# Kernel optimization log

Hardware: AMD Instinct MI355X
Metric: run time of the kernel (lower is better)

Reference implementation:

```python
import jax, jax.numpy as jnp
import numpy as np

NPOINT = 1024   # npoint
K = 20          # num_samples[0]


def _fps(pts, npoint):
    """Iterative furthest point sampling. pts: [N,3] -> indices [npoint] (starts at idx 0)."""
    N = pts.shape[0]

    def step(carry, _):
        min_d, last = carry
        d = jnp.sum((pts - pts[last]) ** 2, axis=-1)          # [N] dist to last selected
        min_d = jnp.minimum(min_d, d)                          # running min-dist to selected set
        nxt = jnp.argmax(min_d).astype(jnp.int32)
        return (min_d, nxt), nxt

    init = (jnp.full((N,), 1e10, pts.dtype), jnp.int32(0))
    _, rest = jax.lax.scan(step, init, None, length=npoint - 1)
    return jnp.concatenate([jnp.zeros((1,), jnp.int32), rest])


def _pdist2(q, p):
    """Squared pairwise distances. q:[M,3], p:[N,3] -> [M,N], clamped to >=0 (matches pdist2squared)."""
    d = jnp.sum(q * q, -1)[:, None] + jnp.sum(p * p, -1)[None, :] - 2.0 * (q @ p.T)
    return jnp.maximum(d, 0.0)


def _knn(q, p, k):
    """k nearest neighbors of each q among p, dropping the closest (self), ascending order."""
    d = _pdist2(q, p)                       # [M,N]
    _, idx = jax.lax.top_k(-d, k + 1)       # ascending distance order
    return idx[:, 1:]                       # drop self, [M,k]


def setup_inputs() -> dict:
    key = jax.random.key(0)
    points = jax.random.normal(key, (4, 16384, 3), dtype=jnp.float32)
    return {"points": points}


def reference(points):
    B, N, _ = points.shape
    # --- FPS node sampling (Sample module) ---
    xyz_ind = jax.vmap(lambda p: _fps(p, NPOINT))(points)                  # [B, N1]
    xyz_query = jnp.take_along_axis(points, xyz_ind[:, :, None], axis=1)  # [B, N1, 3]

    # --- Gmid: neighbors of the N1 query points among all N points ---
    nbr_mid = jax.vmap(lambda q, p: _knn(q, p, K))(xyz_query, points)      # [B, N1, K]
    src_mid = jnp.take_along_axis(points, nbr_mid.reshape(B, -1, 1), axis=1).reshape(B, NPOINT, K, 3)
    d_mid = xyz_query[:, :, None, :] - src_mid                             # edata['d'] = pos[dst]-pos[src]

    # --- Gout: neighbors among the downsampled N1 points themselves ---
    nbr_out = jax.vmap(lambda q: _knn(q, q, K))(xyz_query)                 # [B, N1, K]
    src_out = jnp.take_along_axis(xyz_query, nbr_out.reshape(B, -1, 1), axis=1).reshape(B, NPOINT, K, 3)
    d_out = xyz_query[:, :, None, :] - src_out

    return xyz_ind, xyz_query, nbr_mid, d_mid, nbr_out, d_out
```

## Files before the change

kernel.cpp:

```cpp
#include <hip/hip_runtime.h>
#include <stdint.h>

#define BATCH   4
#define NPTS    16384
#define NPOINT  1024
#define KNN     20
#define KSEL    21

typedef unsigned long long u64;

#define FPS_SUBS 16
#define FPS_TPB  256
#define FPS_BLOCKS (BATCH * FPS_SUBS)
#define FPS_GT   (FPS_SUBS * FPS_TPB)
#define FPS_PPT  (NPTS / FPS_GT)
#define KNN_BLOCKS (BATCH * NPOINT / 4)

#define REPEAT4(M) M(0) M(1) M(2) M(3)

#define FPS_DECL(i) float px##i, py##i, pz##i, md##i;

#define FPS_INIT(i) { \
    int idx = (i) * FPS_GT + g; \
    px##i = P[idx * 3 + 0]; \
    py##i = P[idx * 3 + 1]; \
    pz##i = P[idx * 3 + 2]; \
    md##i = 1e10f; }

#define FPS_STEP(i) { \
    float dx = __fsub_rn(px##i, qx); \
    float dy = __fsub_rn(py##i, qy); \
    float dz = __fsub_rn(pz##i, qz); \
    float d  = __fadd_rn(__fadd_rn(__fmul_rn(dx, dx), __fmul_rn(dy, dy)), \
                         __fmul_rn(dz, dz)); \
    float m = fminf(md##i, d); \
    md##i = m; \
    bool g2 = (m > best); \
    best = g2 ? m : best; \
    bi   = g2 ? (i) : bi; }

__global__ __launch_bounds__(FPS_TPB)
void fused_kernel(const float* __restrict__ pts, float* __restrict__ out,
                  int* __restrict__ ws_ind, float* __restrict__ ws_query,
                  u64* __restrict__ slots,
                  float* __restrict__ out_nbr_mid,
                  float* __restrict__ out_d_mid) {
  __shared__ float s_val[FPS_TPB / 64];
  __shared__ int   s_idx[FPS_TPB / 64];
  __shared__ int   s_widx;

  if (blockIdx.x < FPS_BLOCKS) {
    const int blk = blockIdx.x;
    const int b   = blk >> 4;
    const int sub = blk & 15;
    const int t   = threadIdx.x;
    const int g   = sub * FPS_TPB + t;
    const float* P = pts + (size_t)b * NPTS * 3;
    float* out_ind = out;
    float* out_q   = out + BATCH * NPOINT;

    REPEAT4(FPS_DECL)
    REPEAT4(FPS_INIT)

    if (sub == 0 && t == 0) {
      out_ind[b * NPOINT] = 0.0f;
      ws_ind[b * NPOINT]  = 0;
      float ax = P[0], ay = P[1], az = P[2];
      size_t o0 = (size_t)(b * NPOINT) * 3;
      out_q[o0 + 0] = ax; out_q[o0 + 1] = ay; out_q[o0 + 2] = az;
      ws_query[o0 + 0] = ax; ws_query[o0 + 1] = ay; ws_query[o0 + 2] = az;
    }
    float qx = P[0], qy = P[1], qz = P[2];

    for (int it = 1; it < NPOINT; ++it) {
      float best = -1.0f;
      int bi = 0;
      REPEAT4(FPS_STEP)
      int bidx = bi * FPS_GT + g;

#pragma unroll
      for (int off = 32; off >= 1; off >>= 1) {
        float ov = __shfl_down(best, off);
        int   oi = __shfl_down(bidx, off);
        if (ov > best || (ov == best && oi < bidx)) { best = ov; bidx = oi; }
      }
      if ((t & 63) == 0) { s_val[t >> 6] = best; s_idx[t >> 6] = bidx; }
      __syncthreads();

      if (t < 64) {
        float bv = s_val[0];
        int   bx = s_idx[0];
#pragma unroll
        for (int w = 1; w < FPS_TPB / 64; ++w) {
          float v = s_val[w];
          int   x = s_idx[w];
          if (v > bv || (v == bv && x < bx)) { bv = v; bx = x; }
        }
        u64* row = slots + (size_t)it * (BATCH * FPS_SUBS) + b * FPS_SUBS;
        if (t == 0) {
          u64 pv = ((u64)__float_as_uint(bv) << 32) |
                   (unsigned)(bx | (it << 20));
          __hip_atomic_store(&row[sub], pv, __ATOMIC_RELAXED,
                             __HIP_MEMORY_SCOPE_AGENT);
        }
        int j = t & 15;
        u64 v;
        do {
          v = __hip_atomic_load(&row[j], __ATOMIC_RELAXED,
                                __HIP_MEMORY_SCOPE_AGENT);
        } while ((v >> 63) != 0 ||
                 (((unsigned)(v >> 20)) & 0x3FFu) != (unsigned)it);
        float fv = __uint_as_float((unsigned)(v >> 32));
        int   fi = (int)((unsigned)v & 0xFFFFFu);
#pragma unroll
        for (int off = 8; off >= 1; off >>= 1) {
          float ofv = __shfl_down(fv, off);
          int   ofi = __shfl_down(fi, off);
          if (ofv > fv || (ofv == fv && ofi < fi)) { fv = ofv; fi = ofi; }
        }
        if (t == 0) s_widx = fi;
      }
      __syncthreads();
      const int widx = s_widx;

      qx = P[widx * 3 + 0];
      qy = P[widx * 3 + 1];
      qz = P[widx * 3 + 2];

      if (sub == 0 && t == 0) {
        out_ind[b * NPOINT + it] = (float)widx;
        ws_ind[b * NPOINT + it]  = widx;
        size_t o = (size_t)(b * NPOINT + it) * 3;
        out_q[o + 0] = qx; out_q[o + 1] = qy; out_q[o + 2] = qz;
        ws_query[o + 0] = qx; ws_query[o + 1] = qy; ws_query[o + 2] = qz;
      }
    }
  } else {
#pragma clang fp contract(off)
    const int wv   = (blockIdx.x - FPS_BLOCKS) * 4 + (threadIdx.x >> 6);
    const int lane = threadIdx.x & 63;
    const int b    = wv / NPOINT;
    const int qi   = wv % NPOINT;
    const float* C = pts + (size_t)b * NPTS * 3;

    int widx = 0;
    if (qi > 0) {
      u64* row = slots + (size_t)qi * (BATCH * FPS_SUBS) + b * FPS_SUBS;
      int j = lane & 15;
      u64 v;
      for (;;) {
        v = __hip_atomic_load(&row[j], __ATOMIC_RELAXED,
                              __HIP_MEMORY_SCOPE_AGENT);
        bool ok = ((v >> 63) == 0) &&
                  ((((unsigned)(v >> 20)) & 0x3FFu) == (unsigned)qi);
        if (__all(ok)) break;
        __builtin_amdgcn_s_sleep(64);
      }
      float fv = __uint_as_float((unsigned)(v >> 32));
      int   fi = (int)((unsigned)v & 0xFFFFFu);
#pragma unroll
      for (int off = 8; off >= 1; off >>= 1) {
        float ofv = __shfl_down(fv, off);
        int   ofi = __shfl_down(fi, off);
        if (ofv > fv || (ofv == fv && ofi < fi)) { fv = ofv; fi = ofi; }
      }
      widx = __shfl(fi, 0);
    }

    const float qx = C[widx * 3 + 0];
    const float qy = C[widx * 3 + 1];
    const float qz = C[widx * 3 + 2];
    const float qq = (qx * qx + qy * qy) + qz * qz;

    u64 best[KSEL];
#pragma unroll
    for (int j = 0; j < KSEL; ++j) best[j] = 0xFFFFFFFFFFFFFFFFull;

    for (int j = lane; j < NPTS; j += 64) {
      float px = C[j * 3 + 0], py = C[j * 3 + 1], pz = C[j * 3 + 2];
      float pp  = (px * px + py * py) + pz * pz;
      float dot = __builtin_fmaf(qz, pz, __builtin_fmaf(qy, py, qx * px));
      float d = (qq + pp) - 2.0f * dot;
      d = fmaxf(d, 0.0f);
      u64 key = ((u64)__float_as_uint(d) << 32) | (unsigned)j;
      if (key < best[KSEL - 1]) {
        u64 c = key;
#pragma unroll
        for (int s = 0; s < KSEL; ++s) {
          u64 o = best[s];
          bool l = c < o;
          u64 nb = l ? c : o;
          c = l ? o : c;
          best[s] = nb;
        }
      }
    }

    int hp = 1;
    u64 head = best[0];
    int myK = -1, myIdx = 0;
#pragma unroll
    for (int r = 0; r < KSEL; ++r) {
      u64 v = head; int src = lane;
#pragma unroll
      for (int off = 32; off >= 1; off >>= 1) {
        u64 ov = __shfl_down(v, off);
        int os = __shfl_down(src, off);
        if (ov < v) { v = ov; src = os; }
      }
      v   = __shfl(v, 0);
      src = __shfl(src, 0);
      if (r >= 1 && lane == r - 1) {
        myIdx = (int)(unsigned)(v & 0xFFFFFFFFull);
        myK = r - 1;
      }
      if (lane == src) {
        u64 h = 0xFFFFFFFFFFFFFFFFull;
#pragma unroll
        for (int s = 1; s < KSEL; ++s) if (hp == s) h = best[s];
        head = h;
        hp++;
      }
    }

    if (myK >= 0) {
      size_t o = (size_t)(b * NPOINT + qi) * KNN + myK;
      out_nbr_mid[o] = (float)myIdx;
      float sx = C[myIdx * 3 + 0], sy = C[myIdx * 3 + 1],
            sz = C[myIdx * 3 + 2];
      out_d_mid[o * 3 + 0] = qx - sx;
      out_d_mid[o * 3 + 1] = qy - sy;
      out_d_mid[o * 3 + 2] = qz - sz;
    }
  }
}

#define KNN_WAVES 4

__global__ __launch_bounds__(256)
void knn_kernel(const float* __restrict__ cand_base,
                const float* __restrict__ query_base,
                int ncand,
                float* __restrict__ out_nbr,
                float* __restrict__ out_d) {
#pragma clang fp contract(off)
  const int wid_in_blk = threadIdx.x >> 6;
  const int w    = blockIdx.x * KNN_WAVES + wid_in_blk;
  const int lane = threadIdx.x & 63;
  const int b    = w / NPOINT;
  const int qi   = w % NPOINT;

  const float* C = cand_base + (size_t)b * ncand * 3;
  const float* Q = query_base + ((size_t)b * NPOINT + qi) * 3;
  const float qx = Q[0], qy = Q[1], qz = Q[2];
  const float qq = (qx * qx + qy * qy) + qz * qz;

  u64 best[KSEL];
#pragma unroll
  for (int j = 0; j < KSEL; ++j) best[j] = 0xFFFFFFFFFFFFFFFFull;

  for (int j = lane; j < ncand; j += 64) {
    float px = C[j * 3 + 0], py = C[j * 3 + 1], pz = C[j * 3 + 2];
    float pp  = (px * px + py * py) + pz * pz;
    float dot = __builtin_fmaf(qz, pz, __builtin_fmaf(qy, py, qx * px));
    float d = (qq + pp) - 2.0f * dot;
    d = fmaxf(d, 0.0f);
    u64 key = ((u64)__float_as_uint(d) << 32) | (unsigned)j;
    if (key < best[KSEL - 1]) {
      u64 c = key;
#pragma unroll
      for (int s = 0; s < KSEL; ++s) {
        u64 o = best[s];
        bool l = c < o;
        u64 nb = l ? c : o;
        c = l ? o : c;
        best[s] = nb;
      }
    }
  }

  __shared__ u64 s_list[KNN_WAVES][64 * KSEL];
  u64* L = s_list[wid_in_blk];
#pragma unroll
  for (int j = 0; j < KSEL; ++j) L[lane * KSEL + j] = best[j];
  __syncthreads();

  int hp = 0;
  int myK = -1, myIdx = 0;
  for (int r = 0; r < KSEL; ++r) {
    u64 v = L[lane * KSEL + hp];
    int src = lane;
#pragma unroll
    for (int off = 32; off >= 1; off >>= 1) {
      u64 ov = __shfl_down(v, off);
      int os = __shfl_down(src, off);
      if (ov < v) { v = ov; src = os; }
    }
    v   = __shfl(v, 0);
    src = __shfl(src, 0);
    if (lane == src) hp++;
    if (r >= 1 && lane == r - 1) {
      myIdx = (int)(unsigned)(v & 0xFFFFFFFFull);
      myK = r - 1;
    }
  }

  if (myK >= 0) {
    size_t o = (size_t)(b * NPOINT + qi) * KNN + myK;
    out_nbr[o] = (float)myIdx;
    float sx = C[myIdx * 3 + 0], sy = C[myIdx * 3 + 1], sz = C[myIdx * 3 + 2];
    out_d[o * 3 + 0] = qx - sx;
    out_d[o * 3 + 1] = qy - sy;
    out_d[o * 3 + 2] = qz - sz;
  }
}

extern "C" void kernel_launch(void* const* d_in, const int* in_sizes, int n_in,
                              void* d_out, int out_size, void* d_ws,
                              size_t ws_size, hipStream_t stream) {
  (void)in_sizes; (void)n_in; (void)out_size; (void)ws_size;
  const float* pts = (const float*)d_in[0];
  float* out = (float*)d_out;

  int*   ws_ind   = (int*)d_ws;
  float* ws_query = (float*)((char*)d_ws + (size_t)BATCH * NPOINT * sizeof(int));
  u64*   slots    = (u64*)((char*)d_ws + 64 * 1024);

  float* out_nbr_mid = out + (size_t)BATCH * NPOINT * 4;
  float* out_d_mid   = out_nbr_mid + (size_t)BATCH * NPOINT * KNN;
  float* out_nbr_out = out_d_mid + (size_t)BATCH * NPOINT * KNN * 3;
  float* out_d_out   = out_nbr_out + (size_t)BATCH * NPOINT * KNN;

  hipLaunchKernelGGL(fused_kernel, dim3(FPS_BLOCKS + KNN_BLOCKS),
                     dim3(FPS_TPB), 0, stream,
                     pts, out, ws_ind, ws_query, slots,
                     out_nbr_mid, out_d_mid);

  hipLaunchKernelGGL(knn_kernel, dim3(BATCH * NPOINT / KNN_WAVES), dim3(256),
                     0, stream, ws_query, ws_query, NPOINT, out_nbr_out,
                     out_d_out);
}
```

Before: 2.737 ms.

## Run FPS with one wavefront per block across more blocks, dropping block barriers

```diff
diff --git a/kernel.cpp b/kernel.cpp
--- a/kernel.cpp
+++ b/kernel.cpp
@@ -9,14 +9,14 @@
 
 typedef unsigned long long u64;
 
-#define FPS_SUBS 16
-#define FPS_TPB  256
+#define FPS_SUBS   32
+#define FPS_TPB    256
 #define FPS_BLOCKS (BATCH * FPS_SUBS)
-#define FPS_GT   (FPS_SUBS * FPS_TPB)
-#define FPS_PPT  (NPTS / FPS_GT)
+#define FPS_GT     (FPS_SUBS * 64)
+#define FPS_PPT    (NPTS / FPS_GT)
 #define KNN_BLOCKS (BATCH * NPOINT / 4)
 
-#define REPEAT4(M) M(0) M(1) M(2) M(3)
+#define REPEAT8(M) M(0) M(1) M(2) M(3) M(4) M(5) M(6) M(7)
 
 #define FPS_DECL(i) float px##i, py##i, pz##i, md##i;
 
@@ -45,24 +45,21 @@
                   u64* __restrict__ slots,
                   float* __restrict__ out_nbr_mid,
                   float* __restrict__ out_d_mid) {
-  __shared__ float s_val[FPS_TPB / 64];
-  __shared__ int   s_idx[FPS_TPB / 64];
-  __shared__ int   s_widx;
-
   if (blockIdx.x < FPS_BLOCKS) {
-    const int blk = blockIdx.x;
-    const int b   = blk >> 4;
-    const int sub = blk & 15;
-    const int t   = threadIdx.x;
-    const int g   = sub * FPS_TPB + t;
+    if (threadIdx.x >= 64) return;
+    const int blk  = blockIdx.x;
+    const int b    = blk >> 5;
+    const int sub  = blk & 31;
+    const int lane = threadIdx.x;
+    const int g    = sub * 64 + lane;
     const float* P = pts + (size_t)b * NPTS * 3;
     float* out_ind = out;
     float* out_q   = out + BATCH * NPOINT;
 
-    REPEAT4(FPS_DECL)
-    REPEAT4(FPS_INIT)
-
-    if (sub == 0 && t == 0) {
+    REPEAT8(FPS_DECL)
+    REPEAT8(FPS_INIT)
+
+    if (sub == 0 && lane == 0) {
       out_ind[b * NPOINT] = 0.0f;
       ws_ind[b * NPOINT]  = 0;
       float ax = P[0], ay = P[1], az = P[2];
@@ -75,7 +72,7 @@
     for (int it = 1; it < NPOINT; ++it) {
       float best = -1.0f;
       int bi = 0;
-      REPEAT4(FPS_STEP)
+      REPEAT8(FPS_STEP)
       int bidx = bi * FPS_GT + g;
 
 #pragma unroll
@@ -84,50 +81,36 @@
         int   oi = __shfl_down(bidx, off);
         if (ov > best || (ov == best && oi < bidx)) { best = ov; bidx = oi; }
       }
-      if ((t & 63) == 0) { s_val[t >> 6] = best; s_idx[t >> 6] = bidx; }
-      __syncthreads();
-
-      if (t < 64) {
-        float bv = s_val[0];
-        int   bx = s_idx[0];
-#pragma unroll
-        for (int w = 1; w < FPS_TPB / 64; ++w) {
-          float v = s_val[w];
-          int   x = s_idx[w];
-          if (v > bv || (v == bv && x < bx)) { bv = v; bx = x; }
-        }
-        u64* row = slots + (size_t)it * (BATCH * FPS_SUBS) + b * FPS_SUBS;
-        if (t == 0) {
-          u64 pv = ((u64)__float_as_uint(bv) << 32) |
-                   (unsigned)(bx | (it << 20));
-          __hip_atomic_store(&row[sub], pv, __ATOMIC_RELAXED,
-                             __HIP_MEMORY_SCOPE_AGENT);
-        }
-        int j = t & 15;
-        u64 v;
-        do {
-          v = __hip_atomic_load(&row[j], __ATOMIC_RELAXED,
-                                __HIP_MEMORY_SCOPE_AGENT);
-        } while ((v >> 63) != 0 ||
-                 (((unsigned)(v >> 20)) & 0x3FFu) != (unsigned)it);
-        float fv = __uint_as_float((unsigned)(v >> 32));
-        int   fi = (int)((unsigned)v & 0xFFFFFu);
-#pragma unroll
-        for (int off = 8; off >= 1; off >>= 1) {
-          float ofv = __shfl_down(fv, off);
-          int   ofi = __shfl_down(fi, off);
-          if (ofv > fv || (ofv == fv && ofi < fi)) { fv = ofv; fi = ofi; }
-        }
-        if (t == 0) s_widx = fi;
-      }
-      __syncthreads();
-      const int widx = s_widx;
+
+      u64* row = slots + (size_t)it * (BATCH * FPS_SUBS) + b * FPS_SUBS;
+      if (lane == 0) {
+        u64 pv = ((u64)__float_as_uint(best) << 32) |
+                 (unsigned)(bidx | (it << 20));
+        __hip_atomic_store(&row[sub], pv, __ATOMIC_RELAXED,
+                           __HIP_MEMORY_SCOPE_AGENT);
+      }
+      int j = lane & 31;
+      u64 v;
+      do {
+        v = __hip_atomic_load(&row[j], __ATOMIC_RELAXED,
+                              __HIP_MEMORY_SCOPE_AGENT);
+      } while ((v >> 63) != 0 ||
+               (((unsigned)(v >> 20)) & 0x3FFu) != (unsigned)it);
+      float fv = __uint_as_float((unsigned)(v >> 32));
+      int   fi = (int)((unsigned)v & 0xFFFFFu);
+#pragma unroll
+      for (int off = 32; off >= 1; off >>= 1) {
+        float ofv = __shfl_down(fv, off);
+        int   ofi = __shfl_down(fi, off);
+        if (ofv > fv || (ofv == fv && ofi < fi)) { fv = ofv; fi = ofi; }
+      }
+      const int widx = __shfl(fi, 0);
 
       qx = P[widx * 3 + 0];
       qy = P[widx * 3 + 1];
       qz = P[widx * 3 + 2];
 
-      if (sub == 0 && t == 0) {
+      if (sub == 0 && lane == 0) {
         out_ind[b * NPOINT + it] = (float)widx;
         ws_ind[b * NPOINT + it]  = widx;
         size_t o = (size_t)(b * NPOINT + it) * 3;
@@ -146,7 +129,7 @@
     int widx = 0;
     if (qi > 0) {
       u64* row = slots + (size_t)qi * (BATCH * FPS_SUBS) + b * FPS_SUBS;
-      int j = lane & 15;
+      int j = lane & 31;
       u64 v;
       for (;;) {
         v = __hip_atomic_load(&row[j], __ATOMIC_RELAXED,
@@ -159,7 +142,7 @@
       float fv = __uint_as_float((unsigned)(v >> 32));
       int   fi = (int)((unsigned)v & 0xFFFFFu);
 #pragma unroll
-      for (int off = 8; off >= 1; off >>= 1) {
+      for (int off = 32; off >= 1; off >>= 1) {
         float ofv = __shfl_down(fv, off);
         int   ofi = __shfl_down(fi, off);
         if (ofv > fv || (ofv == fv && ofi < fi)) { fv = ofv; fi = ofi; }
```

New measurement: 3.523 ms. 28.7% more time.
